# Kernel optimization log

Measured on AMD Instinct MI355X. Metric: run time of the kernel, lower is better.

## Reference

```python
import jax, jax.numpy as jnp
import numpy as np

INV_SQRT_4PI = 0.28209479177387814  # 1/sqrt(4*pi)

def sh_l(r, l):
    """Real spherical harmonics of unit vectors r [..., 3], e3nn order,
    'integral' normalization (e3nn o3.spherical_harmonics default)."""
    x, y, z = r[..., 0], r[..., 1], r[..., 2]
    if l == 0:
        return jnp.full(r.shape[:-1] + (1,), INV_SQRT_4PI, r.dtype)
    if l == 1:
        return 0.4886025119029199 * r  # sqrt(3/(4pi)) * (x, y, z)
    s15 = 3.872983346207417 * INV_SQRT_4PI   # sqrt(15)/sqrt(4pi)
    s5 = 2.23606797749979 * INV_SQRT_4PI     # sqrt(5)/sqrt(4pi)
    return jnp.stack([
        s15 * x * z,
        s15 * x * y,
        s5 * (y * y - 0.5 * (x * x + z * z)),
        s15 * y * z,
        0.5 * s15 * (z * z - x * x),
    ], axis=-1)

def layer_norm(x, g, b, eps=1e-5):
    mu = jnp.mean(x, axis=-1, keepdims=True)
    var = jnp.mean((x - mu) ** 2, axis=-1, keepdims=True)
    return (x - mu) * jax.lax.rsqrt(var + eps) * g + b

def setup_inputs() -> dict:
    key = jax.random.key(0)
    N, C, L = 1024, 128, 3  # nodes, sphere_channels, lmax+1
    ks = jax.random.split(key, 12)
    s = 0.02
    return {
        "x_emb": jax.random.normal(ks[0], (N, 9, C), jnp.float32),
        "pos": jax.random.normal(ks[1], (N, 3), jnp.float32) * 3.0,
        "q_w": jax.random.normal(ks[2], (C, C), jnp.float32) * s,
        "q_b": jnp.zeros((C,), jnp.float32),
        "k_w": jax.random.normal(ks[3], (C, C), jnp.float32) * s,
        "k_b": jnp.zeros((C,), jnp.float32),
        "v_w": jax.random.normal(ks[4], (L, C, C), jnp.float32) * s,
        "v_b0": jnp.zeros((C,), jnp.float32),
        "out_w": jax.random.normal(ks[5], (L, C, C), jnp.float32) * s,
        "ln_g": jnp.ones((L, C), jnp.float32),
        "ln_b": jnp.zeros((L, C), jnp.float32),
        "batch": jnp.sort(jax.random.randint(ks[6], (N,), 0, 16)).astype(jnp.int64),
    }

def reference(x_emb, pos, q_w, q_b, k_w, k_b, v_w, v_b0, out_w, ln_g, ln_b, batch):
    N, _, C = x_emb.shape
    H = 8
    D = C // H
    degs = (1, 3, 5)  # 2l+1 for l = 0, 1, 2

    # pairwise unit displacements  [N, N, 3]
    diff = pos[:, None, :] - pos[None, :, :]
    dist = jnp.maximum(jnp.linalg.norm(diff, axis=-1, keepdims=True), 1e-8)
    r_hat = diff / dist

    same = batch[:, None] == batch[None, :]           # [N, N]
    valid = same & ~jnp.eye(N, dtype=bool)

    # per-degree features: split x_emb[:, 9, C] into [1, 3, 5]
    feats = [x_emb[:, 0:1], x_emb[:, 1:4], x_emb[:, 4:9]]

    # HTR invariant pairwise score  [N, N, C]
    score = jnp.zeros((N, N, C), x_emb.dtype)
    for l, f in enumerate(feats):
        sh = sh_l(r_hat, l)                           # [N, N, 2l+1]
        score = score + jnp.einsum('imc,ijm->ijc', f, sh) / degs[l]
    score = score * valid[..., None].astype(score.dtype)

    q = (score.mean(axis=1) @ q_w.T + q_b).reshape(N, H, D)
    k = (score.mean(axis=0) @ k_w.T + k_b).reshape(N, H, D)

    attn = jnp.einsum('ihd,jhd->hij', q, k) * (D ** -0.5)
    attn = jnp.where(same[None], attn, -jnp.inf)
    attn = jnp.nan_to_num(jax.nn.softmax(attn, axis=-1))

    outs = []
    for l, f in enumerate(feats):
        m = degs[l]
        v = f @ v_w[l].T
        if l == 0:
            v = v + v_b0
        v = v.reshape(N, m, H, D)
        o = jnp.einsum('hij,jmhd->imhd', attn, v).reshape(N, m, C)
        o = o @ out_w[l].T
        outs.append(layer_norm(f + o, ln_g[l], ln_b[l]))
    return jnp.concatenate(outs, axis=1)
```

## Files before the change

### kernel.cpp

```cpp
#include <hip/hip_runtime.h>
#include <hip/hip_bf16.h>
#include <math.h>

#define NN 1024

typedef __attribute__((ext_vector_type(8))) short bf16x8;
typedef __attribute__((ext_vector_type(4))) float f32x4;

__device__ __forceinline__ float wave_sum(float v) {
#pragma unroll
  for (int off = 32; off > 0; off >>= 1) v += __shfl_down(v, off);
  return v;
}
__device__ __forceinline__ float wave_max(float v) {
#pragma unroll
  for (int off = 32; off > 0; off >>= 1) v = fmaxf(v, __shfl_down(v, off));
  return v;
}
__device__ __forceinline__ short f2bf(float x) {
  __hip_bfloat16 b = __float2bfloat16(x);
  return *(short*)&b;
}

#define SH_C0 0.28209479177387814f
#define SH_C1 0.4886025119029199f
#define SH_S15 1.0925484305920792f
#define SH_S5 0.6307831305050401f

__global__ __launch_bounds__(256) void htr_geom(
    const float* __restrict__ qw, const float* __restrict__ kw,
    const float* __restrict__ vw, const float* __restrict__ ow,
    const float* __restrict__ x_emb, const float* __restrict__ pos,
    const int* __restrict__ batch, short* __restrict__ wbf,
    short* __restrict__ x_bf, short* __restrict__ fT,
    short* __restrict__ Wsh, short* __restrict__ rowm_bf) {
  const int b = blockIdx.x;
  const int tid = threadIdx.x;
  __shared__ short tile[128][34];
  __shared__ float red[4][9];
  __shared__ float sm[9];

  if (b < 8) {
    const float* src;
    if (b == 0) src = qw;
    else if (b == 1) src = kw;
    else if (b < 5) src = vw + (b - 2) * 16384;
    else src = ow + (b - 5) * 16384;
    short* dst = wbf + b * 16384;
    for (int idx = tid; idx < 16384; idx += 256) dst[idx] = f2bf(src[idx]);
  } else if (b < 1160) {
    int base = (b - 8) * 1024 + tid * 4;
    float4 v = *(const float4*)(x_emb + base);
    *(short4*)(x_bf + base) = make_short4(f2bf(v.x), f2bf(v.y), f2bf(v.z), f2bf(v.w));
  } else if (b < 1448) {
    const int sub = b - 1160;
    const int i0 = (sub & 31) * 32;
    const int m = sub >> 5;
#pragma unroll
    for (int it = 0; it < 16; ++it) {
      int e = tid + it * 256;
      int r = e >> 7, c = e & 127;
      tile[c][r] = f2bf(x_emb[((i0 + r) * 9 + m) * 128 + c]);
    }
    __syncthreads();
#pragma unroll
    for (int it = 0; it < 8; ++it) {
      int idx = tid + it * 256;
      int c = idx >> 4, ii2 = idx & 15;
      *(short2*)(fT + c * 9216 + m * 1024 + i0 + ii2 * 2) =
          make_short2(tile[c][ii2 * 2], tile[c][ii2 * 2 + 1]);
    }
  } else if (b < 2472) {
    const int j = b - 1448;
    const float pjx = pos[j * 3 + 0], pjy = pos[j * 3 + 1], pjz = pos[j * 3 + 2];
    const int bj = batch[j];
    short* wrow = Wsh + j * 9216;
    for (int i = tid; i < 1024; i += 256) {
      float dx = pos[i * 3 + 0] - pjx;
      float dy = pos[i * 3 + 1] - pjy;
      float dz = pos[i * 3 + 2] - pjz;
      bool ok = (i != j) && (batch[i] == bj);
      float okf = ok ? 1.f : 0.f;
      float d2 = dx * dx + dy * dy + dz * dz;
      float inv = okf / fmaxf(sqrtf(d2), 1e-8f);
      float x = dx * inv, y = dy * inv, z = dz * inv;
      wrow[0 * 1024 + i] = f2bf(SH_C0 * okf);
      wrow[1 * 1024 + i] = f2bf((SH_C1 * (1.f / 3.f)) * x);
      wrow[2 * 1024 + i] = f2bf((SH_C1 * (1.f / 3.f)) * y);
      wrow[3 * 1024 + i] = f2bf((SH_C1 * (1.f / 3.f)) * z);
      wrow[4 * 1024 + i] = f2bf((SH_S15 * 0.2f) * x * z);
      wrow[5 * 1024 + i] = f2bf((SH_S15 * 0.2f) * x * y);
      wrow[6 * 1024 + i] = f2bf((SH_S5 * 0.2f) * (y * y - 0.5f * (x * x + z * z)));
      wrow[7 * 1024 + i] = f2bf((SH_S15 * 0.2f) * y * z);
      wrow[8 * 1024 + i] = f2bf((0.5f * SH_S15 * 0.2f) * (z * z - x * x));
    }
  } else {
    const int i = b - 2472;
    const float px = pos[i * 3 + 0], py = pos[i * 3 + 1], pz = pos[i * 3 + 2];
    const int bi = batch[i];
    float s[9];
#pragma unroll
    for (int m = 0; m < 9; ++m) s[m] = 0.f;
    for (int j = tid; j < NN; j += 256) {
      if (j == i) continue;
      if (batch[j] != bi) continue;
      float dx = px - pos[j * 3 + 0];
      float dy = py - pos[j * 3 + 1];
      float dz = pz - pos[j * 3 + 2];
      float d2 = dx * dx + dy * dy + dz * dz;
      float inv = 1.0f / fmaxf(sqrtf(d2), 1e-8f);
      float x = dx * inv, y = dy * inv, z = dz * inv;
      s[0] += 1.0f;
      s[1] += x; s[2] += y; s[3] += z;
      s[4] += x * z; s[5] += x * y;
      s[6] += y * y - 0.5f * (x * x + z * z);
      s[7] += y * z;
      s[8] += z * z - x * x;
    }
    const int wave = tid >> 6, lane = tid & 63;
#pragma unroll
    for (int m = 0; m < 9; ++m) {
      float v = wave_sum(s[m]);
      if (lane == 0) red[wave][m] = v;
    }
    __syncthreads();
    if (tid < 9) {
      float v = red[0][tid] + red[1][tid] + red[2][tid] + red[3][tid];
      float scl = SH_S15 * 0.2f;
      if (tid == 0) scl = SH_C0;
      else if (tid < 4) scl = SH_C1 * (1.f / 3.f);
      else if (tid == 6) scl = SH_S5 * 0.2f;
      else if (tid == 8) scl = 0.5f * SH_S15 * 0.2f;
      sm[tid] = v * scl * (1.0f / 1024.0f);
    }
    __syncthreads();
    if (tid < 128) {
      float acc = 0.f;
#pragma unroll
      for (int m = 0; m < 9; ++m)
        acc = fmaf(sm[m], x_emb[(i * 9 + m) * 128 + tid], acc);
      rowm_bf[i * 128 + tid] = f2bf(acc);
    }
  }
}

#define CMS 16
__global__ __launch_bounds__(64) void htr_colmean_mfma(
    const short* __restrict__ Wsh, const short* __restrict__ fT,
    float* __restrict__ part) {
  const int jbase = blockIdx.x * 16;
  const int ks = blockIdx.y;
  const int lane = threadIdx.x;
  const int q = lane >> 4, l15 = lane & 15;
  const short* ap = Wsh + (jbase + l15) * 9216 + ks * 576 + q * 8;
  const short* bp = fT + l15 * 9216 + ks * 576 + q * 8;
  f32x4 acc[8];
#pragma unroll
  for (int t = 0; t < 8; ++t) acc[t] = (f32x4){0.f, 0.f, 0.f, 0.f};
  bf16x8 a = *(const bf16x8*)ap;
  bf16x8 b[8];
#pragma unroll
  for (int t = 0; t < 8; ++t) b[t] = *(const bf16x8*)(bp + t * 147456);
  for (int s = 1; s < 18; ++s) {
    const int off = s * 32;
    bf16x8 an = *(const bf16x8*)(ap + off);
    bf16x8 bn[8];
#pragma unroll
    for (int t = 0; t < 8; ++t) bn[t] = *(const bf16x8*)(bp + t * 147456 + off);
#pragma unroll
    for (int t = 0; t < 8; ++t)
      acc[t] = __builtin_amdgcn_mfma_f32_16x16x32_bf16(a, b[t], acc[t], 0, 0, 0);
    a = an;
#pragma unroll
    for (int t = 0; t < 8; ++t) b[t] = bn[t];
  }
#pragma unroll
  for (int t = 0; t < 8; ++t)
    acc[t] = __builtin_amdgcn_mfma_f32_16x16x32_bf16(a, b[t], acc[t], 0, 0, 0);
#pragma unroll
  for (int t = 0; t < 8; ++t)
#pragma unroll
    for (int r = 0; r < 4; ++r)
      part[(ks * 1024 + jbase + q * 4 + r) * 128 + t * 16 + l15] = acc[t][r];
}

__global__ __launch_bounds__(64) void htr_proj(
    const short* __restrict__ rowm_bf, const float* __restrict__ part,
    const short* __restrict__ x_bf, const short* __restrict__ wbf,
    const float* __restrict__ q_b, const float* __restrict__ k_b,
    const float* __restrict__ v_b0, float* __restrict__ qbuf,
    float* __restrict__ khbuf, short* __restrict__ vbT) {
  const int ibase = blockIdx.x * 16;
  const int y = blockIdx.y;
  const int lane = threadIdx.x;
  const int q = lane >> 4, l15 = lane & 15;

  bf16x8 a[4];
  const short* bp;
  if (y == 0) {
    const short* ap = rowm_bf + (ibase + l15) * 128 + q * 8;
#pragma unroll
    for (int ks = 0; ks < 4; ++ks) a[ks] = *(const bf16x8*)(ap + ks * 32);
    bp = wbf + l15 * 128 + q * 8;
  } else if (y == 1) {
    const float* pp = part + (size_t)(ibase + l15) * 128;
#pragma unroll
    for (int ks = 0; ks < 4; ++ks) {
      float s0 = 0.f, s1 = 0.f, s2 = 0.f, s3 = 0.f;
      float s4 = 0.f, s5 = 0.f, s6 = 0.f, s7 = 0.f;
#pragma unroll
      for (int s = 0; s < CMS; ++s) {
        const float* ps = pp + s * 131072 + ks * 32 + q * 8;
        float4 u0 = *(const float4*)(ps);
        float4 u1 = *(const float4*)(ps + 4);
        s0 += u0.x; s1 += u0.y; s2 += u0.z; s3 += u0.w;
        s4 += u1.x; s5 += u1.y; s6 += u1.z; s7 += u1.w;
      }
      const float sc = 1.0f / 1024.0f;
      bf16x8 av;
      av[0] = f2bf(s0 * sc); av[1] = f2bf(s1 * sc);
      av[2] = f2bf(s2 * sc); av[3] = f2bf(s3 * sc);
      av[4] = f2bf(s4 * sc); av[5] = f2bf(s5 * sc);
      av[6] = f2bf(s6 * sc); av[7] = f2bf(s7 * sc);
      a[ks] = av;
    }
    bp = wbf + 16384 + l15 * 128 + q * 8;
  } else {
    const int m = y - 2;
    const int l = (m == 0) ? 0 : ((m < 4) ? 1 : 2);
    const short* ap = x_bf + ((ibase + l15) * 9 + m) * 128 + q * 8;
#pragma unroll
    for (int ks = 0; ks < 4; ++ks) a[ks] = *(const bf16x8*)(ap + ks * 32);
    bp = wbf + (2 + l) * 16384 + l15 * 128 + q * 8;
  }

  f32x4 acc[8];
#pragma unroll
  for (int t = 0; t < 8; ++t) {
    acc[t] = (f32x4){0.f, 0.f, 0.f, 0.f};
    const short* bt = bp + t * 2048;
#pragma unroll
    for (int ks = 0; ks < 4; ++ks) {
      bf16x8 b = *(const bf16x8*)(bt + ks * 32);
      acc[t] = __builtin_amdgcn_mfma_f32_16x16x32_bf16(a[ks], b, acc[t], 0, 0, 0);
    }
  }

  if (y == 0) {
#pragma unroll
    for (int t = 0; t < 8; ++t) {
      float bo = q_b[t * 16 + l15];
#pragma unroll
      for (int r = 0; r < 4; ++r)
        qbuf[(ibase + q * 4 + r) * 128 + t * 16 + l15] = acc[t][r] + bo;
    }
  } else if (y == 1) {
#pragma unroll
    for (int t = 0; t < 8; ++t) {
      float bo = k_b[t * 16 + l15];
#pragma unroll
      for (int r = 0; r < 4; ++r)
        khbuf[(t * 1024 + ibase + q * 4 + r) * 16 + l15] = acc[t][r] + bo;
    }
  } else {
    const int m = y - 2;
#pragma unroll
    for (int t = 0; t < 8; ++t) {
      float bias = (m == 0) ? v_b0[t * 16 + l15] : 0.f;
#pragma unroll
      for (int r = 0; r < 4; ++r)
        vbT[(t * 144 + m * 16 + l15) * 1024 + ibase + q * 4 + r] =
            f2bf(acc[t][r] + bias);
    }
  }
}

__global__ __launch_bounds__(256) void htr_attn8(
    const float* __restrict__ qbuf, const float* __restrict__ khbuf,
    const int* __restrict__ batch, short* __restrict__ attn) {
  const int ibase = blockIdx.x * 8;
  const int h = blockIdx.y;
  const int tid = threadIdx.x;
  const int g = tid >> 7;
  const int lj = tid & 127;
  const int i0 = ibase + g * 4;
  float qr[4][16];
  int bi[4];
#pragma unroll
  for (int r = 0; r < 4; ++r) {
    bi[r] = batch[i0 + r];
#pragma unroll
    for (int d = 0; d < 16; ++d)
      qr[r][d] = qbuf[(i0 + r) * 128 + h * 16 + d] * 0.25f;
  }
  float s[4][8];
#pragma unroll
  for (int jt = 0; jt < 8; ++jt) {
    int j = jt * 128 + lj;
    int bj = batch[j];
    const float4* kp = (const float4*)(khbuf + (h * 1024 + j) * 16);
    float4 k0 = kp[0], k1 = kp[1], k2 = kp[2], k3 = kp[3];
#pragma unroll
    for (int r = 0; r < 4; ++r) {
      float d = 0.f;
      d = fmaf(qr[r][0], k0.x, d);  d = fmaf(qr[r][1], k0.y, d);
      d = fmaf(qr[r][2], k0.z, d);  d = fmaf(qr[r][3], k0.w, d);
      d = fmaf(qr[r][4], k1.x, d);  d = fmaf(qr[r][5], k1.y, d);
      d = fmaf(qr[r][6], k1.z, d);  d = fmaf(qr[r][7], k1.w, d);
      d = fmaf(qr[r][8], k2.x, d);  d = fmaf(qr[r][9], k2.y, d);
      d = fmaf(qr[r][10], k2.z, d); d = fmaf(qr[r][11], k2.w, d);
      d = fmaf(qr[r][12], k3.x, d); d = fmaf(qr[r][13], k3.y, d);
      d = fmaf(qr[r][14], k3.z, d); d = fmaf(qr[r][15], k3.w, d);
      s[r][jt] = (bj == bi[r]) ? d : -INFINITY;
    }
  }
  const int wig = (tid >> 6) & 1, lane = tid & 63;
  __shared__ float redm[2][4][2], reds[2][4][2];
#pragma unroll
  for (int r = 0; r < 4; ++r) {
    float mx = s[r][0];
#pragma unroll
    for (int jt = 1; jt < 8; ++jt) mx = fmaxf(mx, s[r][jt]);
    mx = wave_max(mx);
    if (lane == 0) redm[g][r][wig] = mx;
  }
  __syncthreads();
  float M[4];
#pragma unroll
  for (int r = 0; r < 4; ++r) M[r] = fmaxf(redm[g][r][0], redm[g][r][1]);
#pragma unroll
  for (int r = 0; r < 4; ++r) {
    float t = 0.f;
#pragma unroll
    for (int jt = 0; jt < 8; ++jt) {
      s[r][jt] = expf(s[r][jt] - M[r]);
      t += s[r][jt];
    }
    t = wave_sum(t);
    if (lane == 0) reds[g][r][wig] = t;
  }
  __syncthreads();
#pragma unroll
  for (int r = 0; r < 4; ++r) {
    float inv = 1.0f / (reds[g][r][0] + reds[g][r][1]);
    short* dp = attn + (h * 1024 + i0 + r) * 1024;
#pragma unroll
    for (int jt = 0; jt < 8; ++jt) dp[jt * 128 + lj] = f2bf(s[r][jt] * inv);
  }
}

template <int NT0, int NT>
__device__ __forceinline__ void apply_body(
    const short* __restrict__ attn, const short* __restrict__ vbT,
    short* __restrict__ obuf_bf, int ibase, int h, int lane) {
  const int q = lane >> 4, l15 = lane & 15;
  const short* ap = attn + (h * 1024 + ibase + l15) * 1024 + q * 8;
  const short* bp = vbT + (h * 144 + l15) * 1024 + q * 8;
  f32x4 acc[NT];
#pragma unroll
  for (int t = 0; t < NT; ++t) acc[t] = (f32x4){0.f, 0.f, 0.f, 0.f};
  bf16x8 a = *(const bf16x8*)ap;
  bf16x8 b[NT];
#pragma unroll
  for (int t = 0; t < NT; ++t) b[t] = *(const bf16x8*)(bp + (NT0 + t) * 16384);
  for (int ks = 1; ks < 32; ++ks) {
    const int off = ks * 32;
    bf16x8 an = *(const bf16x8*)(ap + off);
    bf16x8 bn[NT];
#pragma unroll
    for (int t = 0; t < NT; ++t)
      bn[t] = *(const bf16x8*)(bp + (NT0 + t) * 16384 + off);
#pragma unroll
    for (int t = 0; t < NT; ++t)
      acc[t] = __builtin_amdgcn_mfma_f32_16x16x32_bf16(a, b[t], acc[t], 0, 0, 0);
    a = an;
#pragma unroll
    for (int t = 0; t < NT; ++t) b[t] = bn[t];
  }
#pragma unroll
  for (int t = 0; t < NT; ++t)
    acc[t] = __builtin_amdgcn_mfma_f32_16x16x32_bf16(a, b[t], acc[t], 0, 0, 0);
#pragma unroll
  for (int t = 0; t < NT; ++t)
#pragma unroll
    for (int r = 0; r < 4; ++r)
      obuf_bf[((ibase + q * 4 + r) * 9 + NT0 + t) * 128 + h * 16 + l15] =
          f2bf(acc[t][r]);
}

__global__ __launch_bounds__(64) void htr_apply_mfma(
    const short* __restrict__ attn, const short* __restrict__ vbT,
    short* __restrict__ obuf_bf) {
  const int ibase = blockIdx.x * 16;
  const int h = blockIdx.y;
  if (blockIdx.z == 0)
    apply_body<0, 5>(attn, vbT, obuf_bf, ibase, h, threadIdx.x);
  else
    apply_body<5, 4>(attn, vbT, obuf_bf, ibase, h, threadIdx.x);
}

__global__ __launch_bounds__(64) void htr_outln_mfma(
    const short* __restrict__ obuf_bf, const float* __restrict__ x_emb,
    const short* __restrict__ wbf, const float* __restrict__ ln_g,
    const float* __restrict__ ln_b, float* __restrict__ out) {
  const int ibase = blockIdx.x * 16;
  const int m = blockIdx.y;
  const int l = (m == 0) ? 0 : ((m < 4) ? 1 : 2);
  const int lane = threadIdx.x;
  const int q = lane >> 4, l15 = lane & 15;
  const short* ap = obuf_bf + ((ibase + l15) * 9 + m) * 128 + q * 8;
  const short* bp = wbf + (5 + l) * 16384 + l15 * 128 + q * 8;
  bf16x8 a[4];
#pragma unroll
  for (int ks = 0; ks < 4; ++ks) a[ks] = *(const bf16x8*)(ap + ks * 32);
  f32x4 acc[8];
#pragma unroll
  for (int t = 0; t < 8; ++t) {
    acc[t] = (f32x4){0.f, 0.f, 0.f, 0.f};
    const short* bt = bp + t * 2048;
#pragma unroll
    for (int ks = 0; ks < 4; ++ks) {
      bf16x8 b = *(const bf16x8*)(bt + ks * 32);
      acc[t] = __builtin_amdgcn_mfma_f32_16x16x32_bf16(a[ks], b, acc[t], 0, 0, 0);
    }
  }
  float g[8], bb[8];
#pragma unroll
  for (int t = 0; t < 8; ++t) {
    g[t] = ln_g[l * 128 + t * 16 + l15];
    bb[t] = ln_b[l * 128 + t * 16 + l15];
  }
#pragma unroll
  for (int r = 0; r < 4; ++r) {
    const int i = ibase + q * 4 + r;
    const float* xr = x_emb + (i * 9 + m) * 128;
    float v[8];
    float sv = 0.f, sq = 0.f;
#pragma unroll
    for (int t = 0; t < 8; ++t) {
      v[t] = acc[t][r] + xr[t * 16 + l15];
      sv += v[t];
      sq += v[t] * v[t];
    }
#pragma unroll
    for (int off = 1; off < 16; off <<= 1) {
      sv += __shfl_xor(sv, off);
      sq += __shfl_xor(sq, off);
    }
    float mu = sv * (1.f / 128.f);
    float var = sq * (1.f / 128.f) - mu * mu;
    float rs = rsqrtf(var + 1e-5f);
    float* orow = out + (i * 9 + m) * 128;
#pragma unroll
    for (int t = 0; t < 8; ++t)
      orow[t * 16 + l15] = (v[t] - mu) * rs * g[t] + bb[t];
  }
}

extern "C" void kernel_launch(void* const* d_in, const int* in_sizes, int n_in,
                              void* d_out, int out_size, void* d_ws, size_t ws_size,
                              hipStream_t stream) {
  (void)in_sizes; (void)n_in; (void)out_size; (void)ws_size;
  const float* x_emb = (const float*)d_in[0];
  const float* pos   = (const float*)d_in[1];
  const float* q_w   = (const float*)d_in[2];
  const float* q_b   = (const float*)d_in[3];
  const float* k_w   = (const float*)d_in[4];
  const float* k_b   = (const float*)d_in[5];
  const float* v_w   = (const float*)d_in[6];
  const float* v_b0  = (const float*)d_in[7];
  const float* out_w = (const float*)d_in[8];
  const float* ln_g  = (const float*)d_in[9];
  const float* ln_b  = (const float*)d_in[10];
  const int*   batch = (const int*)d_in[11];
  float* out = (float*)d_out;

  float* ws = (float*)d_ws;
  short* rowm_bf = (short*)(ws + 0);
  float* qbuf    = ws + 65536;
  float* khbuf   = ws + 196608;
  short* wbf     = (short*)(ws + 327680);
  short* x_bf    = (short*)(ws + 393216);
  short* vbT     = (short*)(ws + 983040);
  short* obuf_bf = (short*)(ws + 1572864);
  short* attn    = (short*)(ws + 2162688);
  float* part    = ws + 2162688;
  short* Wsh     = (short*)(ws + 6356992);
  short* fT      = (short*)(ws + 11075584);

  htr_geom<<<3496, 256, 0, stream>>>(q_w, k_w, v_w, out_w, x_emb, pos, batch,
                                     wbf, x_bf, fT, Wsh, rowm_bf);
  htr_colmean_mfma<<<dim3(64, CMS), 64, 0, stream>>>(Wsh, fT, part);
  htr_proj<<<dim3(64, 11), 64, 0, stream>>>(rowm_bf, part, x_bf, wbf, q_b, k_b,
                                            v_b0, qbuf, khbuf, vbT);
  htr_attn8<<<dim3(128, 8), 256, 0, stream>>>(qbuf, khbuf, batch, attn);
  htr_apply_mfma<<<dim3(64, 8, 2), 64, 0, stream>>>(attn, vbT, obuf_bf);
  htr_outln_mfma<<<dim3(64, 9), 64, 0, stream>>>(obuf_bf, x_emb, wbf, ln_g,
                                                 ln_b, out);
}
```

Measured before the change: 173.5 us.

## Fuse softmax attention and value apply into one kernel via shared memory

Merges the softmax kernel and the attention-times-V MFMA kernel. Each block handles 16 query rows for one head, writes the normalized bf16 probabilities into an XOR-swizzled 32KB LDS tile, and then its four waves split the 9 value components for the MFMA product. This drops the global round trip of the 16MB attention matrix and one kernel launch. In exchange each block is larger, LDS use lowers occupancy, there are fewer blocks (512), and the per-wave MFMA work is uneven (3 vs 2 tiles).

```diff
diff --git a/kernel.cpp b/kernel.cpp
--- a/kernel.cpp
+++ b/kernel.cpp
@@ -275,29 +275,72 @@
   }
 }
 
-__global__ __launch_bounds__(256) void htr_attn8(
+template <int NT0, int NT>
+__device__ __forceinline__ void apply_phase(
+    const short* P, const short* __restrict__ vbT,
+    short* __restrict__ obuf_bf, int ibase, int h, int lane) {
+  const int q = lane >> 4, l15 = lane & 15;
+  const int xs = (l15 & 7) << 3;
+  const short* pr = P + l15 * 1024;
+  const short* bp = vbT + (h * 144 + l15) * 1024 + q * 8;
+  f32x4 acc[NT];
+#pragma unroll
+  for (int t = 0; t < NT; ++t) acc[t] = (f32x4){0.f, 0.f, 0.f, 0.f};
+  bf16x8 a = *(const bf16x8*)(pr + ((q * 8) ^ xs));
+  bf16x8 b[NT];
+#pragma unroll
+  for (int t = 0; t < NT; ++t) b[t] = *(const bf16x8*)(bp + (NT0 + t) * 16384);
+  for (int ks = 1; ks < 32; ++ks) {
+    const int off = ks * 32;
+    bf16x8 an = *(const bf16x8*)(pr + ((off + q * 8) ^ xs));
+    bf16x8 bn[NT];
+#pragma unroll
+    for (int t = 0; t < NT; ++t)
+      bn[t] = *(const bf16x8*)(bp + (NT0 + t) * 16384 + off);
+#pragma unroll
+    for (int t = 0; t < NT; ++t)
+      acc[t] = __builtin_amdgcn_mfma_f32_16x16x32_bf16(a, b[t], acc[t], 0, 0, 0);
+    a = an;
+#pragma unroll
+    for (int t = 0; t < NT; ++t) b[t] = bn[t];
+  }
+#pragma unroll
+  for (int t = 0; t < NT; ++t)
+    acc[t] = __builtin_amdgcn_mfma_f32_16x16x32_bf16(a, b[t], acc[t], 0, 0, 0);
+#pragma unroll
+  for (int t = 0; t < NT; ++t)
+#pragma unroll
+    for (int r = 0; r < 4; ++r)
+      obuf_bf[((ibase + q * 4 + r) * 9 + NT0 + t) * 128 + h * 16 + l15] =
+          f2bf(acc[t][r]);
+}
+
+__global__ __launch_bounds__(256) void htr_attn_apply(
     const float* __restrict__ qbuf, const float* __restrict__ khbuf,
-    const int* __restrict__ batch, short* __restrict__ attn) {
-  const int ibase = blockIdx.x * 8;
+    const int* __restrict__ batch, const short* __restrict__ vbT,
+    short* __restrict__ obuf_bf) {
+  const int ibase = blockIdx.x * 16;
   const int h = blockIdx.y;
   const int tid = threadIdx.x;
-  const int g = tid >> 7;
-  const int lj = tid & 127;
-  const int i0 = ibase + g * 4;
+  const int w = tid >> 6;
+  const int lane = tid & 63;
+  __shared__ short P[16 * 1024];
+
+  const int r0 = ibase + w * 4;
   float qr[4][16];
   int bi[4];
 #pragma unroll
   for (int r = 0; r < 4; ++r) {
-    bi[r] = batch[i0 + r];
-#pragma unroll
-    for (int d = 0; d < 16; ++d)
-      qr[r][d] = qbuf[(i0 + r) * 128 + h * 16 + d] * 0.25f;
-  }
-  float s[4][8];
-#pragma unroll
-  for (int jt = 0; jt < 8; ++jt) {
-    int j = jt * 128 + lj;
-    int bj = batch[j];
+    bi[r] = batch[r0 + r];
+    const float* qp = qbuf + (r0 + r) * 128 + h * 16;
+#pragma unroll
+    for (int d = 0; d < 16; ++d) qr[r][d] = qp[d] * 0.25f;
+  }
+  float s[4][16];
+#pragma unroll
+  for (int jt = 0; jt < 16; ++jt) {
+    const int j = jt * 64 + lane;
+    const int bj = batch[j];
     const float4* kp = (const float4*)(khbuf + (h * 1024 + j) * 16);
     float4 k0 = kp[0], k1 = kp[1], k2 = kp[2], k3 = kp[3];
 #pragma unroll
@@ -314,89 +357,37 @@
       s[r][jt] = (bj == bi[r]) ? d : -INFINITY;
     }
   }
-  const int wig = (tid >> 6) & 1, lane = tid & 63;
-  __shared__ float redm[2][4][2], reds[2][4][2];
 #pragma unroll
   for (int r = 0; r < 4; ++r) {
     float mx = s[r][0];
 #pragma unroll
-    for (int jt = 1; jt < 8; ++jt) mx = fmaxf(mx, s[r][jt]);
+    for (int jt = 1; jt < 16; ++jt) mx = fmaxf(mx, s[r][jt]);
     mx = wave_max(mx);
-    if (lane == 0) redm[g][r][wig] = mx;
+    mx = __shfl(mx, 0);
+    float t = 0.f;
+#pragma unroll
+    for (int jt = 0; jt < 16; ++jt) {
+      s[r][jt] = expf(s[r][jt] - mx);
+      t += s[r][jt];
+    }
+    t = wave_sum(t);
+    t = __shfl(t, 0);
+    const float inv = 1.0f / t;
+    const int row = w * 4 + r;
+    const int xs = (row & 7) << 3;
+    short* pw = P + row * 1024;
+#pragma unroll
+    for (int jt = 0; jt < 16; ++jt) {
+      const int j = jt * 64 + lane;
+      pw[j ^ xs] = f2bf(s[r][jt] * inv);
+    }
   }
   __syncthreads();
-  float M[4];
-#pragma unroll
-  for (int r = 0; r < 4; ++r) M[r] = fmaxf(redm[g][r][0], redm[g][r][1]);
-#pragma unroll
-  for (int r = 0; r < 4; ++r) {
-    float t = 0.f;
-#pragma unroll
-    for (int jt = 0; jt < 8; ++jt) {
-      s[r][jt] = expf(s[r][jt] - M[r]);
-      t += s[r][jt];
-    }
-    t = wave_sum(t);
-    if (lane == 0) reds[g][r][wig] = t;
-  }
-  __syncthreads();
-#pragma unroll
-  for (int r = 0; r < 4; ++r) {
-    float inv = 1.0f / (reds[g][r][0] + reds[g][r][1]);
-    short* dp = attn + (h * 1024 + i0 + r) * 1024;
-#pragma unroll
-    for (int jt = 0; jt < 8; ++jt) dp[jt * 128 + lj] = f2bf(s[r][jt] * inv);
-  }
-}
-
-template <int NT0, int NT>
-__device__ __forceinline__ void apply_body(
-    const short* __restrict__ attn, const short* __restrict__ vbT,
-    short* __restrict__ obuf_bf, int ibase, int h, int lane) {
-  const int q = lane >> 4, l15 = lane & 15;
-  const short* ap = attn + (h * 1024 + ibase + l15) * 1024 + q * 8;
-  const short* bp = vbT + (h * 144 + l15) * 1024 + q * 8;
-  f32x4 acc[NT];
-#pragma unroll
-  for (int t = 0; t < NT; ++t) acc[t] = (f32x4){0.f, 0.f, 0.f, 0.f};
-  bf16x8 a = *(const bf16x8*)ap;
-  bf16x8 b[NT];
-#pragma unroll
-  for (int t = 0; t < NT; ++t) b[t] = *(const bf16x8*)(bp + (NT0 + t) * 16384);
-  for (int ks = 1; ks < 32; ++ks) {
-    const int off = ks * 32;
-    bf16x8 an = *(const bf16x8*)(ap + off);
-    bf16x8 bn[NT];
-#pragma unroll
-    for (int t = 0; t < NT; ++t)
-      bn[t] = *(const bf16x8*)(bp + (NT0 + t) * 16384 + off);
-#pragma unroll
-    for (int t = 0; t < NT; ++t)
-      acc[t] = __builtin_amdgcn_mfma_f32_16x16x32_bf16(a, b[t], acc[t], 0, 0, 0);
-    a = an;
-#pragma unroll
-    for (int t = 0; t < NT; ++t) b[t] = bn[t];
-  }
-#pragma unroll
-  for (int t = 0; t < NT; ++t)
-    acc[t] = __builtin_amdgcn_mfma_f32_16x16x32_bf16(a, b[t], acc[t], 0, 0, 0);
-#pragma unroll
-  for (int t = 0; t < NT; ++t)
-#pragma unroll
-    for (int r = 0; r < 4; ++r)
-      obuf_bf[((ibase + q * 4 + r) * 9 + NT0 + t) * 128 + h * 16 + l15] =
-          f2bf(acc[t][r]);
-}
-
-__global__ __launch_bounds__(64) void htr_apply_mfma(
-    const short* __restrict__ attn, const short* __restrict__ vbT,
-    short* __restrict__ obuf_bf) {
-  const int ibase = blockIdx.x * 16;
-  const int h = blockIdx.y;
-  if (blockIdx.z == 0)
-    apply_body<0, 5>(attn, vbT, obuf_bf, ibase, h, threadIdx.x);
-  else
-    apply_body<5, 4>(attn, vbT, obuf_bf, ibase, h, threadIdx.x);
+
+  if (w == 0)      apply_phase<0, 3>(P, vbT, obuf_bf, ibase, h, lane);
+  else if (w == 1) apply_phase<3, 2>(P, vbT, obuf_bf, ibase, h, lane);
+  else if (w == 2) apply_phase<5, 2>(P, vbT, obuf_bf, ibase, h, lane);
+  else             apply_phase<7, 2>(P, vbT, obuf_bf, ibase, h, lane);
 }
 
 __global__ __launch_bounds__(64) void htr_outln_mfma(
@@ -483,7 +474,6 @@
   short* x_bf    = (short*)(ws + 393216);
   short* vbT     = (short*)(ws + 983040);
   short* obuf_bf = (short*)(ws + 1572864);
-  short* attn    = (short*)(ws + 2162688);
   float* part    = ws + 2162688;
   short* Wsh     = (short*)(ws + 6356992);
   short* fT      = (short*)(ws + 11075584);
@@ -493,8 +483,8 @@
   htr_colmean_mfma<<<dim3(64, CMS), 64, 0, stream>>>(Wsh, fT, part);
   htr_proj<<<dim3(64, 11), 64, 0, stream>>>(rowm_bf, part, x_bf, wbf, q_b, k_b,
                                             v_b0, qbuf, khbuf, vbT);
-  htr_attn8<<<dim3(128, 8), 256, 0, stream>>>(qbuf, khbuf, batch, attn);
-  htr_apply_mfma<<<dim3(64, 8, 2), 64, 0, stream>>>(attn, vbT, obuf_bf);
+  htr_attn_apply<<<dim3(64, 8), 256, 0, stream>>>(qbuf, khbuf, batch, vbT,
+                                                  obuf_bf);
   htr_outln_mfma<<<dim3(64, 9), 64, 0, stream>>>(obuf_bf, x_emb, wbf, ln_g,
                                                  ln_b, out);
 }
```

Measured after the change: 157.7 us. 9.1% less time.
